# Kernel tuning notes

Measured on AMD Instinct MI355X. Metric: run time of the kernel, lower is better.

## Reference

```python
import jax, jax.numpy as jnp
import numpy as np

B, V, H, R, RULE_DIM, DK, GMLP_H, OUT = 4096, 8, 512, 16, 64, 32, 16, 512
TEMP = float(np.sqrt(DK))  # SelectAttention temperature = sqrt(d_k)
EPS = 1e-10


def gumbel_hard(logits, u, tau=1.0):
    # straight-through hard gumbel-softmax over last axis (F.gumbel_softmax hard=True)
    g = -jnp.log(-jnp.log(u + EPS) + EPS)
    y = jax.nn.softmax((logits + g) / tau, axis=-1)
    hard = jax.nn.one_hot(jnp.argmax(y, axis=-1), y.shape[-1], dtype=y.dtype)
    return hard + y - jax.lax.stop_gradient(y)


def setup_inputs() -> dict:
    key = jax.random.key(0)
    ks = jax.random.split(key, 16)
    s = lambda d: 1.0 / np.sqrt(d)
    return {
        "hidden": jax.random.normal(ks[0], (B, V, H), jnp.float32),
        "u_var": jax.random.uniform(ks[1], (B, V * V), jnp.float32),
        "u_rule": jax.random.uniform(ks[2], (B, R), jnp.float32),
        # variable_rule_select: shared query/key Linear(H, 32)
        "Wq": jax.random.normal(ks[3], (H, DK), jnp.float32) * s(H),
        "bq": jnp.zeros((DK,), jnp.float32),
        "Wk": jax.random.normal(ks[4], (H, DK), jnp.float32) * s(H),
        "bk": jnp.zeros((DK,), jnp.float32),
        # rule embeddings [R, rule_dim]
        "rule_emb": jax.random.normal(ks[5], (R, RULE_DIM), jnp.float32),
        # rule_select_: shared Linear(3H, 32) query, Linear(rule_dim, 32) key
        "Wq2": jax.random.normal(ks[6], (3 * H, DK), jnp.float32) * s(3 * H),
        "bq2": jnp.zeros((DK,), jnp.float32),
        "Wk2": jax.random.normal(ks[7], (RULE_DIM, DK), jnp.float32) * s(RULE_DIM),
        "bk2": jnp.zeros((DK,), jnp.float32),
        # rule_mlp = GroupMLP(2H -> 16 -> input_dim, num=R), GroupLinearLayer has no bias
        "W1": jax.random.normal(ks[8], (R, 2 * H, GMLP_H), jnp.float32) * s(2 * H),
        "W2": jax.random.normal(ks[9], (R, GMLP_H, OUT), jnp.float32) * s(GMLP_H),
    }


def reference(hidden, u_var, u_rule, Wq, bq, Wk, bk, rule_emb, Wq2, bq2, Wk2, bk2, W1, W2):
    b, v, h = hidden.shape
    # variable_rule_select(hidden, hidden): shared Linear projections, bmm scores
    q = hidden @ Wq + bq                                  # [B,V,dk]
    k = hidden @ Wk + bk                                  # [B,V,dk]
    scores = jnp.einsum('bid,bjd->bij', q, k) / TEMP      # [B,V,V]
    # hard gumbel-softmax over flattened V*V pair grid
    mask = gumbel_hard(scores.reshape(b, -1), u_var).reshape(b, v, v)
    mask = mask.transpose(0, 2, 1)                        # mask.permute(0,2,1)
    primary = mask.sum(axis=2)                            # [B,V] one-hot primary variable
    context = mask.sum(axis=1)                            # [B,V] one-hot context variable
    h_p = jnp.einsum('bv,bvh->bh', primary, hidden)       # gather primary slot
    h_c = jnp.einsum('bv,bvh->bh', context, hidden)       # gather context slot
    h_mean = hidden.mean(axis=1)
    # rule_select_: query from concat(primary, context, pooled state) [B,3H]
    q2 = jnp.concatenate([h_p, h_c, h_mean], axis=-1) @ Wq2 + bq2   # [B,dk]
    k2 = rule_emb @ Wk2 + bk2                                        # [R,dk]
    rscores = (q2 @ k2.T) / TEMP                                     # [B,R]
    rmask = gumbel_hard(rscores, u_rule)                             # [B,R] one-hot rule
    # rule_mlp: GroupMLP(2H->16->input_dim) over all rules, then hard dispatch
    comb = jnp.concatenate([h_p, h_c], axis=-1)                      # [B,2H]
    h1 = jax.nn.relu(jnp.einsum('bd,rde->bre', comb, W1))            # [B,R,16]
    rout = jnp.einsum('bre,reo->bro', h1, W2)                        # [B,R,out]
    rule_out = jnp.einsum('br,bro->bo', rmask, rout)                 # [B,out]
    # scatter result back to the selected primary variable slot
    out = primary[:, :, None] * rule_out[:, None, :]                 # [B,V,out]
    return out
```

## Files before the change

### kernel.cpp

```cpp
#include <hip/hip_runtime.h>

#define TEMP 5.656854249492380195f
#define EPSG 1e-10f

#define XSTR 68
#define WSTR 64

__launch_bounds__(256, 2)
__global__ void k1_kernel(const float* __restrict__ hidden,
                          const float* __restrict__ u_var,
                          const float* __restrict__ Wq,
                          const float* __restrict__ bq,
                          const float* __restrict__ Wk,
                          const float* __restrict__ bk,
                          const float* __restrict__ rule_emb,
                          const float* __restrict__ Wk2,
                          const float* __restrict__ bk2,
                          float* __restrict__ k2f,
                          int* __restrict__ selbuf,
                          float* __restrict__ outbuf) {
    const int tid = threadIdx.x;
    const int b0  = blockIdx.x * 8;

    __shared__ float4 smem4[(64 * XSTR + 64 * WSTR) / 4];
    float* smem = reinterpret_cast<float*>(smem4);
    float* xt = smem;
    float* wt = smem + 64 * XSTR;

    if (blockIdx.x == 0) {
        for (int t = tid; t < 512; t += 256) {
            int r = t >> 5, d = t & 31;
            float acc = bk2[d];
            for (int h = 0; h < 64; ++h)
                acc += rule_emb[r * 64 + h] * Wk2[h * 32 + d];
            k2f[t] = acc;
        }
    }

    const int tn = tid & 15;
    const int tm = tid >> 4;

    float4 acc0 = make_float4(0.f, 0.f, 0.f, 0.f);
    float4 acc1 = make_float4(0.f, 0.f, 0.f, 0.f);
    float4 acc2 = make_float4(0.f, 0.f, 0.f, 0.f);
    float4 acc3 = make_float4(0.f, 0.f, 0.f, 0.f);

    for (int c = 0; c < 8; ++c) {
        #pragma unroll
        for (int p = 0; p < 4; ++p) {
            int f   = p * 256 + tid;
            int row = f >> 4;
            int c4  = f & 15;
            int bb  = row >> 3, v = row & 7;
            float4 val = *reinterpret_cast<const float4*>(
                hidden + (size_t)(b0 + bb) * 4096 + v * 512 + c * 64 + c4 * 4);
            *reinterpret_cast<float4*>(&xt[row * XSTR + c4 * 4]) = val;
        }
        #pragma unroll
        for (int p = 0; p < 4; ++p) {
            int f  = p * 256 + tid;
            int k  = f >> 4;
            int n4 = f & 15;
            int h  = c * 64 + k;
            const float* src = (n4 < 8) ? (Wq + h * 32 + n4 * 4)
                                        : (Wk + h * 32 + (n4 - 8) * 4);
            *reinterpret_cast<float4*>(&wt[k * WSTR + n4 * 4]) =
                *reinterpret_cast<const float4*>(src);
        }
        __syncthreads();

        #pragma unroll 4
        for (int k4 = 0; k4 < 16; ++k4) {
            float4 x0 = *reinterpret_cast<const float4*>(&xt[(tm * 4 + 0) * XSTR + k4 * 4]);
            float4 x1 = *reinterpret_cast<const float4*>(&xt[(tm * 4 + 1) * XSTR + k4 * 4]);
            float4 x2 = *reinterpret_cast<const float4*>(&xt[(tm * 4 + 2) * XSTR + k4 * 4]);
            float4 x3 = *reinterpret_cast<const float4*>(&xt[(tm * 4 + 3) * XSTR + k4 * 4]);
            float4 w0 = *reinterpret_cast<const float4*>(&wt[(k4 * 4 + 0) * WSTR + tn * 4]);
            float4 w1 = *reinterpret_cast<const float4*>(&wt[(k4 * 4 + 1) * WSTR + tn * 4]);
            float4 w2 = *reinterpret_cast<const float4*>(&wt[(k4 * 4 + 2) * WSTR + tn * 4]);
            float4 w3 = *reinterpret_cast<const float4*>(&wt[(k4 * 4 + 3) * WSTR + tn * 4]);
            acc0.x += x0.x * w0.x + x0.y * w1.x + x0.z * w2.x + x0.w * w3.x;
            acc0.y += x0.x * w0.y + x0.y * w1.y + x0.z * w2.y + x0.w * w3.y;
            acc0.z += x0.x * w0.z + x0.y * w1.z + x0.z * w2.z + x0.w * w3.z;
            acc0.w += x0.x * w0.w + x0.y * w1.w + x0.z * w2.w + x0.w * w3.w;
            acc1.x += x1.x * w0.x + x1.y * w1.x + x1.z * w2.x + x1.w * w3.x;
            acc1.y += x1.x * w0.y + x1.y * w1.y + x1.z * w2.y + x1.w * w3.y;
            acc1.z += x1.x * w0.z + x1.y * w1.z + x1.z * w2.z + x1.w * w3.z;
            acc1.w += x1.x * w0.w + x1.y * w1.w + x1.z * w2.w + x1.w * w3.w;
            acc2.x += x2.x * w0.x + x2.y * w1.x + x2.z * w2.x + x2.w * w3.x;
            acc2.y += x2.x * w0.y + x2.y * w1.y + x2.z * w2.y + x2.w * w3.y;
            acc2.z += x2.x * w0.z + x2.y * w1.z + x2.z * w2.z + x2.w * w3.z;
            acc2.w += x2.x * w0.w + x2.y * w1.w + x2.z * w2.w + x2.w * w3.w;
            acc3.x += x3.x * w0.x + x3.y * w1.x + x3.z * w2.x + x3.w * w3.x;
            acc3.y += x3.x * w0.y + x3.y * w1.y + x3.z * w2.y + x3.w * w3.y;
            acc3.z += x3.x * w0.z + x3.y * w1.z + x3.z * w2.z + x3.w * w3.z;
            acc3.w += x3.x * w0.w + x3.y * w1.w + x3.z * w2.w + x3.w * w3.w;
        }

        {
            int bb = tid >> 5, hg = tid & 31;
            float m0 = 0.f, m1 = 0.f;
            #pragma unroll
            for (int v = 0; v < 8; ++v) {
                float2 x2 = *reinterpret_cast<const float2*>(&xt[(bb * 8 + v) * XSTR + hg * 2]);
                m0 += x2.x; m1 += x2.y;
            }
            float2 o; o.x = m0 * 0.125f; o.y = m1 * 0.125f;
            *reinterpret_cast<float2*>(outbuf + (size_t)(b0 + bb) * 4096 + c * 64 + hg * 2) = o;
        }
        __syncthreads();
    }

    {
        const float* bsrc = (tn < 8) ? (bq + tn * 4) : (bk + (tn - 8) * 4);
        float4 bias4 = *reinterpret_cast<const float4*>(bsrc);
        float4 r0, r1, r2, r3;
        r0.x = acc0.x + bias4.x; r0.y = acc0.y + bias4.y; r0.z = acc0.z + bias4.z; r0.w = acc0.w + bias4.w;
        r1.x = acc1.x + bias4.x; r1.y = acc1.y + bias4.y; r1.z = acc1.z + bias4.z; r1.w = acc1.w + bias4.w;
        r2.x = acc2.x + bias4.x; r2.y = acc2.y + bias4.y; r2.z = acc2.z + bias4.z; r2.w = acc2.w + bias4.w;
        r3.x = acc3.x + bias4.x; r3.y = acc3.y + bias4.y; r3.z = acc3.z + bias4.z; r3.w = acc3.w + bias4.w;
        float* sq = smem;
        *reinterpret_cast<float4*>(&sq[(tm * 4 + 0) * XSTR + tn * 4]) = r0;
        *reinterpret_cast<float4*>(&sq[(tm * 4 + 1) * XSTR + tn * 4]) = r1;
        *reinterpret_cast<float4*>(&sq[(tm * 4 + 2) * XSTR + tn * 4]) = r2;
        *reinterpret_cast<float4*>(&sq[(tm * 4 + 3) * XSTR + tn * 4]) = r3;
    }
    __syncthreads();

    {
        const float* sq = smem;
        const int w    = tid >> 6;
        const int lane = tid & 63;
        #pragma unroll
        for (int half = 0; half < 2; ++half) {
            const int bb = w + half * 4;
            const int b  = b0 + bb;
            const int i = lane >> 3, j = lane & 7;
            float s = 0.f;
            #pragma unroll
            for (int d4 = 0; d4 < 8; ++d4) {
                float4 qv = *reinterpret_cast<const float4*>(&sq[(bb * 8 + i) * XSTR + d4 * 4]);
                float4 kv = *reinterpret_cast<const float4*>(&sq[(bb * 8 + j) * XSTR + 32 + d4 * 4]);
                s += qv.x * kv.x + qv.y * kv.y + qv.z * kv.z + qv.w * kv.w;
            }
            s /= TEMP;
            float u = u_var[(size_t)b * 64 + lane];
            float g = -logf(-logf(u + EPSG) + EPSG);
            float pm = s + g;
            int idx = lane;
            #pragma unroll
            for (int off = 32; off >= 1; off >>= 1) {
                float pv = __shfl_xor(pm, off);
                int   pi = __shfl_xor(idx, off);
                if (pv > pm || (pv == pm && pi < idx)) { pm = pv; idx = pi; }
            }
            if (lane == 0) selbuf[b] = idx;
        }
    }
}

__launch_bounds__(256, 3)
__global__ void k23_kernel(const float* __restrict__ hidden,
                           const float* __restrict__ u_rule,
                           const float* __restrict__ Wq2,
                           const float* __restrict__ bq2,
                           const float* __restrict__ k2f,
                           const int* __restrict__ selbuf,
                           const float* __restrict__ hmeanbuf,
                           const float* __restrict__ W1,
                           const float* __restrict__ W2,
                           float* __restrict__ outbuf) {
    const int tid = threadIdx.x;
    const int b0  = blockIdx.x * 4;

    __shared__ float  s_k2[512];
    __shared__ float  comb[4][1024];
    __shared__ float  hm[4][512];
    __shared__ float4 part4[4][4][8];
    __shared__ float  s_q2[4][32];
    __shared__ int    s_sel4[4];
    __shared__ int    s_rsel[4];

    s_k2[tid]       = k2f[tid];
    s_k2[tid + 256] = k2f[tid + 256];
    if (tid < 4) s_sel4[tid] = selbuf[b0 + tid];
    __syncthreads();

    {
        const float4* h4 = reinterpret_cast<const float4*>(hidden);
        #pragma unroll
        for (int p = 0; p < 4; ++p) {
            int f   = p * 256 + tid;
            int bb  = f >> 8, idx = f & 255;
            int half = idx >> 7, c = idx & 127;
            int sv  = s_sel4[bb];
            int row = half ? (sv >> 3) : (sv & 7);
            float4 v = h4[((size_t)(b0 + bb) * 8 + row) * 128 + c];
            *reinterpret_cast<float4*>(&comb[bb][idx * 4]) = v;
        }
        #pragma unroll
        for (int p = 0; p < 2; ++p) {
            int f  = p * 256 + tid;
            int bb = f >> 7, c = f & 127;
            float4 v = *reinterpret_cast<const float4*>(
                hmeanbuf + (size_t)(b0 + bb) * 4096 + c * 4);
            *reinterpret_cast<float4*>(&hm[bb][c * 4]) = v;
        }
    }
    __syncthreads();

    {
        const int d4 = tid & 7, s = tid >> 3;
        float4 acc[4];
        #pragma unroll
        for (int bb = 0; bb < 4; ++bb) acc[bb] = make_float4(0.f, 0.f, 0.f, 0.f);

        for (int kt = 0; kt < 6; ++kt) {
            float4 w[8];
            #pragma unroll
            for (int j = 0; j < 8; ++j)
                w[j] = *reinterpret_cast<const float4*>(
                    Wq2 + (size_t)(kt * 256 + s * 8 + j) * 32 + d4 * 4);
            #pragma unroll
            for (int bb = 0; bb < 4; ++bb) {
                const float* xsrc = (kt < 4) ? &comb[bb][kt * 256]
                                             : &hm[bb][(kt - 4) * 256];
                #pragma unroll
                for (int j = 0; j < 8; ++j) {
                    float x = xsrc[s * 8 + j];
                    acc[bb].x += x * w[j].x;
                    acc[bb].y += x * w[j].y;
                    acc[bb].z += x * w[j].z;
                    acc[bb].w += x * w[j].w;
                }
            }
        }
        #pragma unroll
        for (int off = 8; off < 64; off <<= 1) {
            #pragma unroll
            for (int bb = 0; bb < 4; ++bb) {
                acc[bb].x += __shfl_xor(acc[bb].x, off);
                acc[bb].y += __shfl_xor(acc[bb].y, off);
                acc[bb].z += __shfl_xor(acc[bb].z, off);
                acc[bb].w += __shfl_xor(acc[bb].w, off);
            }
        }
        if ((s & 7) == 0) {
            #pragma unroll
            for (int bb = 0; bb < 4; ++bb) part4[tid >> 6][bb][d4] = acc[bb];
        }
    }
    __syncthreads();
    if (tid < 128) {
        const int bb = tid >> 5, col = tid & 31;
        float q2 = bq2[col];
        #pragma unroll
        for (int wv = 0; wv < 4; ++wv) {
            const float* pf = reinterpret_cast<const float*>(&part4[wv][bb][col >> 2]);
            q2 += pf[col & 3];
        }
        s_q2[bb][col] = q2;
    }
    __syncthreads();
    if (tid < 64) {
        const int bb = tid >> 4, r = tid & 15;
        const int b = b0 + bb;
        float sc = 0.f;
        #pragma unroll
        for (int d = 0; d < 32; ++d) sc += s_q2[bb][d] * s_k2[r * 32 + d];
        sc /= TEMP;
        float u = u_rule[(size_t)b * 16 + r];
        float g = -logf(-logf(u + EPSG) + EPSG);
        float pm = sc + g;
        int idx = r;
        #pragma unroll
        for (int off = 8; off >= 1; off >>= 1) {
            float pv = __shfl_xor(pm, off, 16);
            int   pi = __shfl_xor(idx, off, 16);
            if (pv > pm || (pv == pm && pi < idx)) { pm = pv; idx = pi; }
        }
        if (r == 0) s_rsel[bb] = idx;
    }
    __syncthreads();

    {
        const int w    = tid >> 6;
        const int lane = tid & 63;
        const int b    = b0 + w;
        const int sv   = s_sel4[w];
        const int js   = sv & 7;
        const int r    = s_rsel[w];

        const int e  = lane & 15;
        const int sl = lane >> 4;
        const float* cb  = comb[w];
        const float* w1p = W1 + (size_t)r * 16384;
        float a = 0.f;
        for (int i = 0; i < 256; ++i) {
            int rr = i * 4 + sl;
            a += cb[rr] * w1p[rr * 16 + e];
        }
        a += __shfl_xor(a, 16);
        a += __shfl_xor(a, 32);
        a = fmaxf(a, 0.f);

        const float* w2 = W2 + (size_t)r * 8192 + lane * 8;
        float4 oA = make_float4(0.f, 0.f, 0.f, 0.f);
        float4 oB = make_float4(0.f, 0.f, 0.f, 0.f);
        #pragma unroll
        for (int ee = 0; ee < 16; ++ee) {
            float he = __shfl(a, ee);
            float4 wa = *reinterpret_cast<const float4*>(w2 + ee * 512);
            float4 wb = *reinterpret_cast<const float4*>(w2 + ee * 512 + 4);
            oA.x += he * wa.x; oA.y += he * wa.y; oA.z += he * wa.z; oA.w += he * wa.w;
            oB.x += he * wb.x; oB.y += he * wb.y; oB.z += he * wb.z; oB.w += he * wb.w;
        }

        float4 z = make_float4(0.f, 0.f, 0.f, 0.f);
        float* ob = outbuf + (size_t)b * 4096 + lane * 8;
        #pragma unroll
        for (int v = 0; v < 8; ++v) {
            bool hit = (v == js);
            *reinterpret_cast<float4*>(ob + v * 512)     = hit ? oA : z;
            *reinterpret_cast<float4*>(ob + v * 512 + 4) = hit ? oB : z;
        }
    }
}

extern "C" void kernel_launch(void* const* d_in, const int* in_sizes, int n_in,
                              void* d_out, int out_size, void* d_ws, size_t ws_size,
                              hipStream_t stream) {
    const float* hidden   = (const float*)d_in[0];
    const float* u_var    = (const float*)d_in[1];
    const float* u_rule   = (const float*)d_in[2];
    const float* Wq       = (const float*)d_in[3];
    const float* bq       = (const float*)d_in[4];
    const float* Wk       = (const float*)d_in[5];
    const float* bk       = (const float*)d_in[6];
    const float* rule_emb = (const float*)d_in[7];
    const float* Wq2      = (const float*)d_in[8];
    const float* bq2      = (const float*)d_in[9];
    const float* Wk2      = (const float*)d_in[10];
    const float* bk2      = (const float*)d_in[11];
    const float* W1       = (const float*)d_in[12];
    const float* W2       = (const float*)d_in[13];

    char* ws = (char*)d_ws;
    float* k2f  = (float*)(ws);
    int*   sel  = (int*)(ws + 4096);
    float* outf = (float*)d_out;

    hipLaunchKernelGGL(k1_kernel, dim3(512), dim3(256), 0, stream,
                       hidden, u_var, Wq, bq, Wk, bk,
                       rule_emb, Wk2, bk2, k2f, sel, outf);
    hipLaunchKernelGGL(k23_kernel, dim3(1024), dim3(256), 0, stream,
                       hidden, u_rule, Wq2, bq2, k2f, sel, outf, W1, W2, outf);
}
```

Measured before the change: 91.53 us.

## Process rule MLP per batch row with whole block instead of one wave per row

The rule-MLP stage now loops over the block's four batch rows and uses all 256 threads on each row, instead of giving each row a single 64-lane wave. The W1 reduction is split across 16 slices and combined through shared memory, and the W2 projection is staged in shared memory before the output stores. This shortens the serial 256-iteration W1 loop per thread to 64 iterations. In exchange it adds several block-wide barriers per row and serialises the four rows, which costs the overlap between waves.

```diff
diff --git a/kernel.cpp b/kernel.cpp
--- a/kernel.cpp
+++ b/kernel.cpp
@@ -180,6 +180,9 @@
     __shared__ float  s_q2[4][32];
     __shared__ int    s_sel4[4];
     __shared__ int    s_rsel[4];
+    __shared__ float  part[4][16];
+    __shared__ float  s_h1[16];
+    __shared__ float  s_rout[512];
 
     s_k2[tid]       = k2f[tid];
     s_k2[tid + 256] = k2f[tid + 256];
@@ -283,46 +286,63 @@
     }
     __syncthreads();
 
-    {
-        const int w    = tid >> 6;
-        const int lane = tid & 63;
-        const int b    = b0 + w;
-        const int sv   = s_sel4[w];
-        const int js   = sv & 7;
-        const int r    = s_rsel[w];
-
-        const int e  = lane & 15;
-        const int sl = lane >> 4;
-        const float* cb  = comb[w];
-        const float* w1p = W1 + (size_t)r * 16384;
-        float a = 0.f;
-        for (int i = 0; i < 256; ++i) {
-            int rr = i * 4 + sl;
-            a += cb[rr] * w1p[rr * 16 + e];
-        }
-        a += __shfl_xor(a, 16);
-        a += __shfl_xor(a, 32);
-        a = fmaxf(a, 0.f);
-
-        const float* w2 = W2 + (size_t)r * 8192 + lane * 8;
-        float4 oA = make_float4(0.f, 0.f, 0.f, 0.f);
-        float4 oB = make_float4(0.f, 0.f, 0.f, 0.f);
-        #pragma unroll
-        for (int ee = 0; ee < 16; ++ee) {
-            float he = __shfl(a, ee);
-            float4 wa = *reinterpret_cast<const float4*>(w2 + ee * 512);
-            float4 wb = *reinterpret_cast<const float4*>(w2 + ee * 512 + 4);
-            oA.x += he * wa.x; oA.y += he * wa.y; oA.z += he * wa.z; oA.w += he * wa.w;
-            oB.x += he * wb.x; oB.y += he * wb.y; oB.z += he * wb.z; oB.w += he * wb.w;
-        }
-
-        float4 z = make_float4(0.f, 0.f, 0.f, 0.f);
-        float* ob = outbuf + (size_t)b * 4096 + lane * 8;
-        #pragma unroll
-        for (int v = 0; v < 8; ++v) {
-            bool hit = (v == js);
-            *reinterpret_cast<float4*>(ob + v * 512)     = hit ? oA : z;
-            *reinterpret_cast<float4*>(ob + v * 512 + 4) = hit ? oB : z;
+    for (int bb = 0; bb < 4; ++bb) {
+        const int b  = b0 + bb;
+        const int sv = s_sel4[bb];
+        const int r  = s_rsel[bb];
+        const int js = sv & 7;
+
+        {
+            const int e  = tid & 15;
+            const int sl = tid >> 4;
+            const float* cb  = comb[bb];
+            const float* w1p = W1 + (size_t)r * 16384;
+            float a = 0.f;
+            for (int i = 0; i < 64; ++i) {
+                int rr = i * 16 + sl;
+                a += cb[rr] * w1p[rr * 16 + e];
+            }
+            a += __shfl_xor(a, 16);
+            a += __shfl_xor(a, 32);
+            if ((sl & 3) == 0) part[sl >> 2][e] = a;
+        }
+        __syncthreads();
+        if (tid < 16)
+            s_h1[tid] = fmaxf(part[0][tid] + part[1][tid] + part[2][tid] + part[3][tid], 0.f);
+        __syncthreads();
+
+        {
+            const float* w2 = W2 + (size_t)r * 8192;
+            int o0 = tid * 2;
+            float a0 = 0.f, a1 = 0.f;
+            #pragma unroll
+            for (int ee = 0; ee < 16; ++ee) {
+                float h1e = s_h1[ee];
+                float2 ww = *reinterpret_cast<const float2*>(w2 + ee * 512 + o0);
+                a0 += h1e * ww.x;
+                a1 += h1e * ww.y;
+            }
+            s_rout[o0]     = a0;
+            s_rout[o0 + 1] = a1;
+        }
+        __syncthreads();
+
+        {
+            const int v    = tid >> 5;
+            const int col0 = (tid & 31) * 16;
+            float4 z = make_float4(0.f, 0.f, 0.f, 0.f);
+            float4 r0 = z, r1 = z, r2 = z, r3 = z;
+            if (v == js) {
+                r0 = *reinterpret_cast<const float4*>(&s_rout[col0]);
+                r1 = *reinterpret_cast<const float4*>(&s_rout[col0 + 4]);
+                r2 = *reinterpret_cast<const float4*>(&s_rout[col0 + 8]);
+                r3 = *reinterpret_cast<const float4*>(&s_rout[col0 + 12]);
+            }
+            float* ob = outbuf + (size_t)b * 4096 + v * 512 + col0;
+            *reinterpret_cast<float4*>(ob)      = r0;
+            *reinterpret_cast<float4*>(ob + 4)  = r1;
+            *reinterpret_cast<float4*>(ob + 8)  = r2;
+            *reinterpret_cast<float4*>(ob + 12) = r3;
         }
     }
 }
```

New measurement: 128.3 us. 1.4x slower.
